# Kernel optimization log

Hardware: AMD Instinct MI355X
Metric: run time of the kernel (lower is better)

## Reference

```python
import jax, jax.numpy as jnp
import numpy as np

D_IN, H, NH = 256, 512, 8
B, T = 8, 1024


def sinusoidal_pe(seq_len, d_model):
    pos = jnp.arange(seq_len, dtype=jnp.float32)[:, None]
    div = jnp.exp(jnp.arange(0, d_model, 2, dtype=jnp.float32) * (-jnp.log(10000.0) / d_model))
    pe = jnp.zeros((seq_len, d_model), jnp.float32)
    pe = pe.at[:, 0::2].set(jnp.sin(pos * div)).at[:, 1::2].set(jnp.cos(pos * div))
    return pe


def layer_norm(x, g, b, eps=1e-5):
    mu = jnp.mean(x, -1, keepdims=True)
    var = jnp.mean((x - mu) ** 2, -1, keepdims=True)
    return (x - mu) * jax.lax.rsqrt(var + eps) * g + b


def lstm_dir(x, wih, whh, bih, bhh):
    # x: [B,T,H]; wih/whh: [4H,H]; gate order i,f,g,o (PyTorch convention)
    Bx = x.shape[0]
    Hh = whh.shape[1]
    xg = jnp.einsum('bth,gh->btg', x, wih) + bih  # precompute input gates [B,T,4H]

    def step(carry, xg_t):
        h, c = carry
        gates = xg_t + h @ whh.T + bhh
        i, f, g, o = jnp.split(gates, 4, axis=-1)
        c = jax.nn.sigmoid(f) * c + jax.nn.sigmoid(i) * jnp.tanh(g)
        h = jax.nn.sigmoid(o) * jnp.tanh(c)
        return (h, c), h

    h0 = jnp.zeros((Bx, Hh), x.dtype)
    _, hs = jax.lax.scan(step, (h0, h0), xg.transpose(1, 0, 2))
    return hs.transpose(1, 0, 2)  # [B,T,H]


def setup_inputs():
    key = jax.random.key(0)
    ks = jax.random.split(key, 30)
    s = 0.02

    def g(k, shape):
        return jax.random.normal(k, shape, jnp.float32) * s

    return {
        'temporal_data': jax.random.normal(ks[0], (B, T, D_IN), jnp.float32),
        'w_in': g(ks[1], (H, D_IN)), 'b_in': jnp.zeros((H,), jnp.float32),
        'wq': g(ks[2], (H, H)), 'bq': jnp.zeros((H,), jnp.float32),
        'wk': g(ks[3], (H, H)), 'bk': jnp.zeros((H,), jnp.float32),
        'wv': g(ks[4], (H, H)), 'bv': jnp.zeros((H,), jnp.float32),
        'wo': g(ks[5], (H, H)), 'bo': jnp.zeros((H,), jnp.float32),
        'g1': jnp.ones((H,), jnp.float32), 'b1': jnp.zeros((H,), jnp.float32),
        'wih_f': g(ks[6], (4 * H, H)), 'whh_f': g(ks[7], (4 * H, H)),
        'bih_f': jnp.zeros((4 * H,), jnp.float32), 'bhh_f': jnp.zeros((4 * H,), jnp.float32),
        'wih_b': g(ks[8], (4 * H, H)), 'whh_b': g(ks[9], (4 * H, H)),
        'bih_b': jnp.zeros((4 * H,), jnp.float32), 'bhh_b': jnp.zeros((4 * H,), jnp.float32),
        'g2': jnp.ones((2 * H,), jnp.float32), 'b2': jnp.zeros((2 * H,), jnp.float32),
        'w_out': g(ks[10], (H, 2 * H)), 'b_out': jnp.zeros((H,), jnp.float32),
    }


def reference(temporal_data, w_in, b_in, wq, bq, wk, bk, wv, bv, wo, bo, g1, b1,
              wih_f, whh_f, bih_f, bhh_f, wih_b, whh_b, bih_b, bhh_b, g2, b2, w_out, b_out):
    x = temporal_data @ w_in.T + b_in                      # [B,T,H]
    Bx, Tx, _ = x.shape
    x = x + sinusoidal_pe(Tx, H)
    residual = x

    hd = H // NH
    q = (x @ wq.T + bq).reshape(Bx, Tx, NH, hd).transpose(0, 2, 1, 3)
    k = (x @ wk.T + bk).reshape(Bx, Tx, NH, hd).transpose(0, 2, 1, 3)
    v = (x @ wv.T + bv).reshape(Bx, Tx, NH, hd).transpose(0, 2, 1, 3)
    scores = jnp.einsum('bhqd,bhkd->bhqk', q, k) * (hd ** -0.5)
    causal = jnp.triu(jnp.ones((Tx, Tx), bool), 1)
    scores = jnp.where(causal, jnp.float32(-1e9), scores)
    attn = jax.nn.softmax(scores, axis=-1)
    o = jnp.einsum('bhqk,bhkd->bhqd', attn, v).transpose(0, 2, 1, 3).reshape(Bx, Tx, H)
    o = o @ wo.T + bo

    x = layer_norm(o + residual, g1, b1)                   # dropout in eval = identity

    h_fwd = lstm_dir(x, wih_f, whh_f, bih_f, bhh_f)
    h_bwd = jnp.flip(lstm_dir(jnp.flip(x, 1), wih_b, whh_b, bih_b, bhh_b), 1)
    lstm_out = jnp.concatenate([h_fwd, h_bwd], axis=-1)    # [B,T,2H]
    lstm_out = layer_norm(lstm_out, g2, b2)

    emb = jnp.mean(lstm_out, axis=1)                       # [B,2H]
    return emb @ w_out.T + b_out                           # [B,H]
```

## Files before the change

### kernel.cpp

```cpp
#include <hip/hip_runtime.h>

typedef unsigned short u16;
typedef unsigned int   u32;
typedef unsigned long long u64;
typedef __attribute__((ext_vector_type(8))) short short8v;
typedef __attribute__((ext_vector_type(4))) float f32x4;
typedef __attribute__((ext_vector_type(4))) unsigned int u32x4;

#define DINL __device__ __forceinline__

DINL u16 f2bf(float f){ union{float f;u32 u;} v{f}; return (u16)((v.u + 0x7fffu + ((v.u>>16)&1u))>>16); }
DINL float bf2f(u16 b){ union{u32 u;float f;} v{(u32)b<<16}; return v.f; }
DINL f32x4 MFMA16(short8v a, short8v b, f32x4 c){ return __builtin_amdgcn_mfma_f32_16x16x32_bf16(a,b,c,0,0,0); }
DINL void gl16(const void* g, void* l){
  __builtin_amdgcn_global_load_lds((const __attribute__((address_space(1))) void*)g,
                                   (__attribute__((address_space(3))) void*)l, 16, 0, 0);
}
DINL float wredd(float v){
#pragma unroll
  for (int m=1;m<64;m<<=1) v += __shfl_xor(v, m);
  return v;
}
DINL float sigm(float x){ return 1.f/(1.f+__expf(-x)); }
DINL float tanh_(float x){ return 2.f/(1.f+__expf(-2.f*x)) - 1.f; }

__global__ __launch_bounds__(256) void zerok(u32* __restrict__ dst){
  size_t i = ((size_t)blockIdx.x*256 + threadIdx.x)*4;
  u32x4 z = {0,0,0,0};
  *(u32x4*)(dst + i) = z;
}

__global__ __launch_bounds__(256) void cvtk(const float* __restrict__ src, u16* __restrict__ dst, int n){
  int i = (blockIdx.x*256 + threadIdx.x)*4;
  float4 v = *(const float4*)(src + i);
  dst[i+0]=f2bf(v.x); dst[i+1]=f2bf(v.y); dst[i+2]=f2bf(v.z); dst[i+3]=f2bf(v.w);
}

template<int EPI>
__global__ __launch_bounds__(256) void gemm128(
    const u16* __restrict__ A, const u16* __restrict__ W,
    const float* __restrict__ bias0, const float* __restrict__ bias1, const float* __restrict__ bias2,
    const u16* __restrict__ resid, u16* __restrict__ out, int M, int N, int K)
{
  __shared__ __align__(16) u16 Al[128*64];
  __shared__ __align__(16) u16 Bl[128*64];
  const int tid = threadIdx.x, lane = tid & 63, w = tid >> 6;
  const int wr = w >> 1, wc = w & 1;
  const int m0 = blockIdx.y * 128, n0 = blockIdx.x * 128;
  f32x4 acc[4][4] = {};
  for (int k0 = 0; k0 < K; k0 += 64) {
#pragma unroll
    for (int j = 0; j < 4; ++j) {
      int idx = (j*4 + w)*64 + lane;
      int r = idx >> 3, c8 = idx & 7;
      gl16(A + (size_t)(m0 + r)*K + k0 + c8*8, (void*)(Al + (size_t)(j*4+w)*512));
      gl16(W + (size_t)(n0 + r)*K + k0 + c8*8, (void*)(Bl + (size_t)(j*4+w)*512));
    }
    __syncthreads();
#pragma unroll
    for (int kk = 0; kk < 2; ++kk) {
      short8v af[4], bf[4];
#pragma unroll
      for (int i = 0; i < 4; ++i)
        af[i] = *(const short8v*)(Al + ((wr*64 + i*16 + (lane&15))*64 + kk*32 + (lane>>4)*8));
#pragma unroll
      for (int i = 0; i < 4; ++i)
        bf[i] = *(const short8v*)(Bl + ((wc*64 + i*16 + (lane&15))*64 + kk*32 + (lane>>4)*8));
#pragma unroll
      for (int mi=0;mi<4;++mi)
#pragma unroll
        for (int ni=0;ni<4;++ni)
          acc[mi][ni] = MFMA16(af[mi], bf[ni], acc[mi][ni]);
    }
    __syncthreads();
  }
#pragma unroll
  for (int mi=0;mi<4;++mi)
#pragma unroll
    for (int ni=0;ni<4;++ni)
#pragma unroll
      for (int r=0;r<4;++r) {
        int m = m0 + wr*64 + mi*16 + (lane>>4)*4 + r;
        int n = n0 + wc*64 + ni*16 + (lane&15);
        float v = acc[mi][ni][r];
        if constexpr (EPI == 0) {
          int t = m & 1023;
          float ang = (float)t * expf((float)(n & ~1) * (-9.210340371976184f/512.f));
          v += bias0[n] + ((n & 1) ? cosf(ang) : sinf(ang));
          out[(size_t)m*512 + n] = f2bf(v);
        } else if constexpr (EPI == 1) {
          int g = n >> 9, n5 = n & 511, hh = n5 >> 6, dh = n5 & 63;
          v += (g==0 ? bias0 : g==1 ? bias1 : bias2)[n5];
          size_t bh = (size_t)((m>>10)*8 + hh);
          u16 val = f2bf(v);
          if (g == 0)      out[(bh*1024 + (m&1023))*64 + dh] = val;
          else if (g == 1) out[4194304 + (bh*1024 + (m&1023))*64 + dh] = val;
          else             out[8388608 + (bh*64 + dh)*1024 + (m&1023)] = val;
        } else {
          v += bias0[n] + bf2f(resid[(size_t)m*512 + n]);
          out[(size_t)m*512 + n] = f2bf(v);
        }
      }
}

__global__ __launch_bounds__(256) void attnk(const u16* __restrict__ qb, const u16* __restrict__ kb,
                                             const u16* __restrict__ vt, u16* __restrict__ attno)
{
  __shared__ __align__(16) u16 P[4][16][72];
  const int tid = threadIdx.x, lane = tid & 63, w = tid >> 6;
  const int bh = blockIdx.x >> 4, qblk = blockIdx.x & 15;
  const int b = bh >> 3, h = bh & 7;
  const float scale = 0.125f;
  short8v qf[2];
  {
    const u16* qbase = qb + ((size_t)bh*1024 + qblk*64 + w*16)*64;
#pragma unroll
    for (int kk=0;kk<2;++kk)
      qf[kk] = *(const short8v*)(qbase + (size_t)(lane&15)*64 + kk*32 + (lane>>4)*8);
  }
  f32x4 o[4] = {};
  float mrun[4], lrun[4];
#pragma unroll
  for (int r=0;r<4;++r){ mrun[r] = -1e30f; lrun[r] = 0.f; }
  for (int kblk = 0; kblk <= qblk; ++kblk) {
    f32x4 s[4] = {};
#pragma unroll
    for (int kk=0;kk<2;++kk)
#pragma unroll
      for (int nt=0;nt<4;++nt) {
        short8v kf = *(const short8v*)(kb + ((size_t)bh*1024 + kblk*64 + nt*16 + (lane&15))*64 + kk*32 + (lane>>4)*8);
        s[nt] = MFMA16(qf[kk], kf, s[nt]);
      }
    float pnew[4][4];
#pragma unroll
    for (int r=0;r<4;++r) {
      int q = qblk*64 + w*16 + (lane>>4)*4 + r;
      float sv[4]; float rowmax = -1e30f;
#pragma unroll
      for (int nt=0;nt<4;++nt) {
        int key = kblk*64 + nt*16 + (lane&15);
        float x = s[nt][r]*scale;
        if (key > q) x = -1e30f;
        sv[nt] = x; rowmax = fmaxf(rowmax, x);
      }
#pragma unroll
      for (int msk=1; msk<16; msk<<=1) rowmax = fmaxf(rowmax, __shfl_xor(rowmax, msk));
      float mnew = fmaxf(mrun[r], rowmax);
      float sf = __expf(mrun[r]-mnew);
      float psum = 0.f;
#pragma unroll
      for (int nt=0;nt<4;++nt){ float p = __expf(sv[nt]-mnew); pnew[nt][r]=p; psum += p; }
#pragma unroll
      for (int msk=1; msk<16; msk<<=1) psum += __shfl_xor(psum, msk);
      lrun[r] = lrun[r]*sf + psum;
      mrun[r] = mnew;
#pragma unroll
      for (int nt=0;nt<4;++nt) o[nt][r] *= sf;
    }
#pragma unroll
    for (int nt=0;nt<4;++nt)
#pragma unroll
      for (int r=0;r<4;++r)
        P[w][(lane>>4)*4+r][nt*16+(lane&15)] = f2bf(pnew[nt][r]);
#pragma unroll
    for (int kk=0;kk<2;++kk) {
      short8v pf = *(const short8v*)&P[w][lane&15][kk*32 + (lane>>4)*8];
#pragma unroll
      for (int nt=0;nt<4;++nt) {
        short8v vf = *(const short8v*)(vt + ((size_t)bh*64 + nt*16 + (lane&15))*1024 + kblk*64 + kk*32 + (lane>>4)*8);
        o[nt] = MFMA16(pf, vf, o[nt]);
      }
    }
  }
#pragma unroll
  for (int nt=0;nt<4;++nt)
#pragma unroll
    for (int r=0;r<4;++r) {
      int q = qblk*64 + w*16 + (lane>>4)*4 + r;
      int dh = nt*16 + (lane&15);
      attno[((size_t)b*1024 + q)*512 + h*64 + dh] = f2bf(o[nt][r] / lrun[r]);
    }
}

__global__ __launch_bounds__(256) void ln1k(const u16* __restrict__ pre, const float* __restrict__ g1,
                                            const float* __restrict__ b1, u16* __restrict__ xl){
  int row = blockIdx.x*4 + (threadIdx.x>>6), lane = threadIdx.x&63;
  short8v xv = *(const short8v*)(pre + (size_t)row*512 + lane*8);
  float v[8], s=0.f, s2=0.f;
#pragma unroll
  for (int e=0;e<8;++e){ v[e]=bf2f((u16)xv[e]); s+=v[e]; s2+=v[e]*v[e]; }
  s = wredd(s); s2 = wredd(s2);
  float mu = s*(1.f/512.f);
  float rs = rsqrtf(s2*(1.f/512.f) - mu*mu + 1e-5f);
  int b = row>>10, t = row&1023;
  short8v ov;
#pragma unroll
  for (int e=0;e<8;++e){ int c=lane*8+e; ov[e]=(short)f2bf((v[e]-mu)*rs*g1[c]+b1[c]); }
  *(short8v*)(xl + ((size_t)t*8 + b)*512 + lane*8) = ov;
}

__global__ __launch_bounds__(512, 2) void lstmk(
    const u16* __restrict__ xl,
    const float* __restrict__ wih_f, const float* __restrict__ whh_f,
    const float* __restrict__ bih_f, const float* __restrict__ bhh_f,
    const float* __restrict__ wih_b, const float* __restrict__ whh_b,
    const float* __restrict__ bih_b, const float* __restrict__ bhh_b,
    u32* __restrict__ hx, u16* __restrict__ hs)
{
  extern __shared__ float RED[];

  const int tid = threadIdx.x, lane = tid&63, w = tid>>6;
  const int d = blockIdx.x >> 4, slice = blockIdx.x & 15, u0 = slice*32;
  const float* WIHg = d ? wih_b : wih_f;
  const float* WHHg = d ? whh_b : whh_f;
  const float* BIH  = d ? bih_b : bih_f;
  const float* BHH  = d ? bhh_b : bhh_f;

  const int l15 = lane&15, l16 = lane>>4;

  short8v wi[8][2], wh[8][2];
#pragma unroll
  for (int nt=0; nt<8; ++nt) {
    const int g = nt>>1, uh = nt&1;
    const size_t row = (size_t)(g*512 + u0 + uh*16 + l15);
#pragma unroll
    for (int kk=0; kk<2; ++kk) {
      const int k = w*64 + kk*32 + l16*8;
      const float* pi = WIHg + row*512 + k;
      const float* ph = WHHg + row*512 + k;
      float4 a0 = *(const float4*)pi, a1 = *(const float4*)(pi+4);
      float4 b0 = *(const float4*)ph, b1 = *(const float4*)(ph+4);
      short8v si, sh;
      si[0]=(short)f2bf(a0.x); si[1]=(short)f2bf(a0.y); si[2]=(short)f2bf(a0.z); si[3]=(short)f2bf(a0.w);
      si[4]=(short)f2bf(a1.x); si[5]=(short)f2bf(a1.y); si[6]=(short)f2bf(a1.z); si[7]=(short)f2bf(a1.w);
      sh[0]=(short)f2bf(b0.x); sh[1]=(short)f2bf(b0.y); sh[2]=(short)f2bf(b0.z); sh[3]=(short)f2bf(b0.w);
      sh[4]=(short)f2bf(b1.x); sh[5]=(short)f2bf(b1.y); sh[6]=(short)f2bf(b1.z); sh[7]=(short)f2bf(b1.w);
      wi[nt][kk] = si; wh[nt][kk] = sh;
    }
  }

  const bool act = tid < 256;
  const int b_ = tid>>5, u_ = tid&31;
  float c_state = 0.f, bias_c[4];
  if (act)
#pragma unroll
    for (int g=0;g<4;++g) bias_c[g] = BIH[g*512+u0+u_] + BHH[g*512+u0+u_];

  __syncthreads();

  for (int t = 0; t < 1024; ++t) {
    const int te = d ? 1023 - t : t;
    f32x4 acc[8] = {};
    {
      const u16* xb = xl + ((size_t)te*8 + (lane&7))*512 + w*64 + l16*8;
      short8v xf0 = *(const short8v*)(xb);
      short8v xf1 = *(const short8v*)(xb + 32);
#pragma unroll
      for (int nt=0; nt<8; ++nt) acc[nt] = MFMA16(xf0, wi[nt][0], acc[nt]);
#pragma unroll
      for (int nt=0; nt<8; ++nt) acc[nt] = MFMA16(xf1, wi[nt][1], acc[nt]);
    }
    if (t > 0) {
      const u32 tg = (u32)t;
      const u32* pb = hx + ((size_t)d*2 + ((t-1)&1))*4096 + (size_t)(lane&7)*512 + w*64 + l16*8;
      u32x4 q0,q1,q2,q3;
      for (;;) {
        asm volatile(
          "global_load_dwordx4 %0, %4, off sc0 sc1\n\t"
          "global_load_dwordx4 %1, %4, off offset:16 sc0 sc1\n\t"
          "global_load_dwordx4 %2, %4, off offset:128 sc0 sc1\n\t"
          "global_load_dwordx4 %3, %4, off offset:144 sc0 sc1\n\t"
          "s_waitcnt vmcnt(0)"
          : "=&v"(q0),"=&v"(q1),"=&v"(q2),"=&v"(q3)
          : "v"(pb));
        bool ok = true;
#pragma unroll
        for (int e=0;e<4;++e) {
          ok = ok && ((q0[e]&0xffffu)==tg) && ((q1[e]&0xffffu)==tg)
                  && ((q2[e]&0xffffu)==tg) && ((q3[e]&0xffffu)==tg);
        }
        if (__all(ok)) break;
        __builtin_amdgcn_s_sleep(1);
      }
      short8v hf0, hf1;
#pragma unroll
      for (int e=0;e<4;++e) {
        hf0[e]   = (short)(q0[e] >> 16);
        hf0[4+e] = (short)(q1[e] >> 16);
        hf1[e]   = (short)(q2[e] >> 16);
        hf1[4+e] = (short)(q3[e] >> 16);
      }
#pragma unroll
      for (int nt=0; nt<8; ++nt) acc[nt] = MFMA16(hf0, wh[nt][0], acc[nt]);
#pragma unroll
      for (int nt=0; nt<8; ++nt) acc[nt] = MFMA16(hf1, wh[nt][1], acc[nt]);
    }
    float* R = RED + (size_t)(t & 1)*8192;
    if (lane < 32)
#pragma unroll
      for (int nt=0; nt<8; ++nt)
        *(f32x4*)(R + ((size_t)(w*8+nt)*32 + lane)*4) = acc[nt];
    __syncthreads();
    if (act) {
      const int lc = (u_&15) + 16*(b_>>2), rg = b_&3, uh = u_>>4;
      float gates[4];
#pragma unroll
      for (int g=0;g<4;++g) {
        float s = 0.f;
#pragma unroll
        for (int wv=0; wv<8; ++wv) s += R[((size_t)(wv*8 + g*2 + uh)*32 + lc)*4 + rg];
        gates[g] = s + bias_c[g];
      }
      float ig = sigm(gates[0]), fg = sigm(gates[1]), gg = tanh_(gates[2]), og = sigm(gates[3]);
      c_state = fg*c_state + ig*gg;
      u16 hv = f2bf(og * tanh_(c_state));
      hs[((size_t)(d*1024 + te)*8 + b_)*512 + u0 + u_] = hv;
      u32 word = ((u32)hv << 16) | (u32)(t + 1);
      u32* dst = hx + ((size_t)d*2 + (t&1))*4096 + (size_t)b_*512 + u0 + u_;
      asm volatile("global_store_dword %0, %1, off sc0 sc1" :: "v"(dst), "v"(word) : "memory");
    }
  }
}

__global__ __launch_bounds__(256) void ln2k(const u16* __restrict__ hs, const float* __restrict__ g2,
                                            const float* __restrict__ b2, float* __restrict__ emb){
  __shared__ float accl[4][1024];
  int b = blockIdx.x>>4, chunk = blockIdx.x&15;
  int lane = threadIdx.x&63, w = threadIdx.x>>6;
  for (int i=lane;i<1024;i+=64) accl[w][i]=0.f;
#pragma unroll 1
  for (int i=0;i<16;++i) {
    int t = chunk*64 + w*16 + i;
    short8v xf = *(const short8v*)(hs + ((size_t)t*8 + b)*512 + lane*8);
    short8v xb = *(const short8v*)(hs + ((size_t)(1024+t)*8 + b)*512 + lane*8);
    float vf[8], vb[8], s=0.f, s2=0.f;
#pragma unroll
    for (int e=0;e<8;++e){ vf[e]=bf2f((u16)xf[e]); vb[e]=bf2f((u16)xb[e]);
                           s += vf[e]+vb[e]; s2 += vf[e]*vf[e]+vb[e]*vb[e]; }
    s = wredd(s); s2 = wredd(s2);
    float mu = s*(1.f/1024.f);
    float rs = rsqrtf(s2*(1.f/1024.f) - mu*mu + 1e-5f);
#pragma unroll
    for (int e=0;e<8;++e){
      int c = lane*8+e;
      accl[w][c]     += (vf[e]-mu)*rs*g2[c]     + b2[c];
      accl[w][512+c] += (vb[e]-mu)*rs*g2[512+c] + b2[512+c];
    }
  }
  __syncthreads();
  for (int c = threadIdx.x; c < 1024; c += 256)
    atomicAdd(emb + (size_t)b*1024 + c, accl[0][c]+accl[1][c]+accl[2][c]+accl[3][c]);
}

__global__ __launch_bounds__(256) void fink(const float* __restrict__ emb, const float* __restrict__ w_out,
                                            const float* __restrict__ b_out, float* __restrict__ out){
  int gid = blockIdx.x*256 + threadIdx.x;
  int n = gid>>3, b = gid&7;
  const float* e = emb + (size_t)b*1024;
  const float* wr = w_out + (size_t)n*1024;
  float s = 0.f;
  for (int k=0;k<1024;k+=4) {
    float4 ev = *(const float4*)(e+k);
    float4 wv = *(const float4*)(wr+k);
    s += ev.x*wv.x + ev.y*wv.y + ev.z*wv.z + ev.w*wv.w;
  }
  out[(size_t)b*512 + n] = b_out[n] + s*(1.f/1024.f);
}

#define OFF_EMB   0u
#define OFF_HX    32768u
#define OFF_A0    98304u
#define OFF_WIN   4292608u
#define OFF_WQKV  4554752u
#define OFF_WO    6127616u
#define OFF_X0B   6651904u
#define OFF_QB    15040512u
#define OFF_PRE   15040512u
#define OFF_XL    23429120u
#define OFF_ATT   40206336u
#define OFF_HS    48594944u

extern "C" void kernel_launch(void* const* d_in, const int* in_sizes, int n_in,
                              void* d_out, int out_size, void* d_ws, size_t ws_size,
                              hipStream_t stream) {
  const float* temporal = (const float*)d_in[0];
  const float* w_in = (const float*)d_in[1];  const float* b_in = (const float*)d_in[2];
  const float* wq = (const float*)d_in[3];    const float* bq = (const float*)d_in[4];
  const float* wk = (const float*)d_in[5];    const float* bk = (const float*)d_in[6];
  const float* wv = (const float*)d_in[7];    const float* bv = (const float*)d_in[8];
  const float* wo = (const float*)d_in[9];    const float* bo = (const float*)d_in[10];
  const float* g1 = (const float*)d_in[11];   const float* b1 = (const float*)d_in[12];
  const float* wih_f = (const float*)d_in[13]; const float* whh_f = (const float*)d_in[14];
  const float* bih_f = (const float*)d_in[15]; const float* bhh_f = (const float*)d_in[16];
  const float* wih_b = (const float*)d_in[17]; const float* whh_b = (const float*)d_in[18];
  const float* bih_b = (const float*)d_in[19]; const float* bhh_b = (const float*)d_in[20];
  const float* g2 = (const float*)d_in[21];   const float* b2 = (const float*)d_in[22];
  const float* w_out = (const float*)d_in[23]; const float* b_out = (const float*)d_in[24];

  char* ws = (char*)d_ws;
  float* EMB = (float*)(ws + OFF_EMB);
  u32* HX   = (u32*)(ws + OFF_HX);
  u16* A0   = (u16*)(ws + OFF_A0);
  u16* WIN  = (u16*)(ws + OFF_WIN);
  u16* WQKV = (u16*)(ws + OFF_WQKV);
  u16* WOb  = (u16*)(ws + OFF_WO);
  u16* X0B  = (u16*)(ws + OFF_X0B);
  u16* QB   = (u16*)(ws + OFF_QB);
  u16* PRE  = (u16*)(ws + OFF_PRE);
  u16* XL   = (u16*)(ws + OFF_XL);
  u16* ATT  = (u16*)(ws + OFF_ATT);
  u16* HS   = (u16*)(ws + OFF_HS);

  (void)hipFuncSetAttribute((const void*)lstmk, hipFuncAttributeMaxDynamicSharedMemorySize, 65536);

  zerok<<<24,256,0,stream>>>((u32*)(ws + OFF_EMB));

  cvtk<<<2048,256,0,stream>>>(temporal, A0, 2097152);
  cvtk<<<128, 256,0,stream>>>(w_in, WIN, 131072);
  cvtk<<<256, 256,0,stream>>>(wq, WQKV,           262144);
  cvtk<<<256, 256,0,stream>>>(wk, WQKV + 262144,  262144);
  cvtk<<<256, 256,0,stream>>>(wv, WQKV + 524288,  262144);
  cvtk<<<256, 256,0,stream>>>(wo, WOb, 262144);

  gemm128<0><<<dim3(4,64), 256, 0, stream>>>(A0, WIN, b_in, nullptr, nullptr, nullptr, X0B, 8192, 512, 256);
  gemm128<1><<<dim3(12,64),256, 0, stream>>>(X0B, WQKV, bq, bk, bv, nullptr, QB, 8192, 1536, 512);
  attnk<<<1024,256,0,stream>>>(QB, QB + 4194304, QB + 8388608, ATT);
  gemm128<3><<<dim3(4,64), 256, 0, stream>>>(ATT, WOb, bo, nullptr, nullptr, X0B, PRE, 8192, 512, 512);
  ln1k<<<2048,256,0,stream>>>(PRE, g1, b1, XL);
  lstmk<<<32,512,65536,stream>>>(XL, wih_f, whh_f, bih_f, bhh_f, wih_b, whh_b, bih_b, bhh_b, HX, HS);
  ln2k<<<128,256,0,stream>>>(HS, g2, b2, EMB);
  fink<<<16,256,0,stream>>>(EMB, w_out, b_out, (float*)d_out);
}
```

Baseline: 3.399 ms.

## Prefetch LSTM hidden-state poll before input MFMAs and pad reduction LDS layout

The first poll of the previous step's hidden-state words is issued as relaxed agent-scope atomic loads before the input-gate MFMAs, so the cross-block exchange latency overlaps compute instead of being serialized after it. The LDS partial-sum layout is changed to a padded stride-9 layout that puts the eight warp partials next to each other, which is meant to cut bank conflicts in the gate reduction, with a tree-shaped sum. The launch bound drops the 2-blocks hint and shared memory grows to fit the padding. Relaxed atomics replace the explicit sc0 sc1 cache-bypass loads, which may change visibility behaviour in the spin loop.

```diff
diff --git a/kernel.cpp b/kernel.cpp
--- a/kernel.cpp
+++ b/kernel.cpp
@@ -199,7 +199,7 @@
   *(short8v*)(xl + ((size_t)t*8 + b)*512 + lane*8) = ov;
 }
 
-__global__ __launch_bounds__(512, 2) void lstmk(
+__global__ __launch_bounds__(512) void lstmk(
     const u16* __restrict__ xl,
     const float* __restrict__ wih_f, const float* __restrict__ whh_f,
     const float* __restrict__ bih_f, const float* __restrict__ bhh_f,
@@ -250,6 +250,15 @@
 
   for (int t = 0; t < 1024; ++t) {
     const int te = d ? 1023 - t : t;
+    u64 pv[8];
+    const u64* pb = (const u64*)(hx + ((size_t)d*2 + ((t-1)&1))*4096
+                                    + (size_t)(lane&7)*512 + w*64 + l16*8);
+    if (t > 0) {
+#pragma unroll
+      for (int j=0;j<4;++j) pv[j]   = __hip_atomic_load(pb+j,    __ATOMIC_RELAXED, __HIP_MEMORY_SCOPE_AGENT);
+#pragma unroll
+      for (int j=0;j<4;++j) pv[4+j] = __hip_atomic_load(pb+16+j, __ATOMIC_RELAXED, __HIP_MEMORY_SCOPE_AGENT);
+    }
     f32x4 acc[8] = {};
     {
       const u16* xb = xl + ((size_t)te*8 + (lane&7))*512 + w*64 + l16*8;
@@ -262,54 +271,46 @@
     }
     if (t > 0) {
       const u32 tg = (u32)t;
-      const u32* pb = hx + ((size_t)d*2 + ((t-1)&1))*4096 + (size_t)(lane&7)*512 + w*64 + l16*8;
-      u32x4 q0,q1,q2,q3;
       for (;;) {
-        asm volatile(
-          "global_load_dwordx4 %0, %4, off sc0 sc1\n\t"
-          "global_load_dwordx4 %1, %4, off offset:16 sc0 sc1\n\t"
-          "global_load_dwordx4 %2, %4, off offset:128 sc0 sc1\n\t"
-          "global_load_dwordx4 %3, %4, off offset:144 sc0 sc1\n\t"
-          "s_waitcnt vmcnt(0)"
-          : "=&v"(q0),"=&v"(q1),"=&v"(q2),"=&v"(q3)
-          : "v"(pb));
         bool ok = true;
 #pragma unroll
-        for (int e=0;e<4;++e) {
-          ok = ok && ((q0[e]&0xffffu)==tg) && ((q1[e]&0xffffu)==tg)
-                  && ((q2[e]&0xffffu)==tg) && ((q3[e]&0xffffu)==tg);
-        }
+        for (int j=0;j<8;++j)
+          ok = ok && ((u32)(pv[j] & 0xffffu) == tg) && ((u32)((pv[j]>>32) & 0xffffu) == tg);
         if (__all(ok)) break;
         __builtin_amdgcn_s_sleep(1);
+#pragma unroll
+        for (int j=0;j<4;++j) pv[j]   = __hip_atomic_load(pb+j,    __ATOMIC_RELAXED, __HIP_MEMORY_SCOPE_AGENT);
+#pragma unroll
+        for (int j=0;j<4;++j) pv[4+j] = __hip_atomic_load(pb+16+j, __ATOMIC_RELAXED, __HIP_MEMORY_SCOPE_AGENT);
       }
       short8v hf0, hf1;
 #pragma unroll
-      for (int e=0;e<4;++e) {
-        hf0[e]   = (short)(q0[e] >> 16);
-        hf0[4+e] = (short)(q1[e] >> 16);
-        hf1[e]   = (short)(q2[e] >> 16);
-        hf1[4+e] = (short)(q3[e] >> 16);
+      for (int j=0;j<4;++j) {
+        hf0[2*j]   = (short)(u32)(pv[j]   >> 16);
+        hf0[2*j+1] = (short)(pv[j]   >> 48);
+        hf1[2*j]   = (short)(u32)(pv[4+j] >> 16);
+        hf1[2*j+1] = (short)(pv[4+j] >> 48);
       }
 #pragma unroll
       for (int nt=0; nt<8; ++nt) acc[nt] = MFMA16(hf0, wh[nt][0], acc[nt]);
 #pragma unroll
       for (int nt=0; nt<8; ++nt) acc[nt] = MFMA16(hf1, wh[nt][1], acc[nt]);
     }
-    float* R = RED + (size_t)(t & 1)*8192;
+    float* R = RED + (size_t)(t & 1)*9216;
     if (lane < 32)
 #pragma unroll
       for (int nt=0; nt<8; ++nt)
-        *(f32x4*)(R + ((size_t)(w*8+nt)*32 + lane)*4) = acc[nt];
+#pragma unroll
+        for (int rg=0; rg<4; ++rg)
+          R[(((size_t)nt*4 + rg)*32 + lane)*9 + w] = acc[nt][rg];
     __syncthreads();
     if (act) {
-      const int lc = (u_&15) + 16*(b_>>2), rg = b_&3, uh = u_>>4;
+      const int uh = u_>>4, lc = (u_&15) + 16*(b_>>2), rg = b_&3;
       float gates[4];
 #pragma unroll
       for (int g=0;g<4;++g) {
-        float s = 0.f;
-#pragma unroll
-        for (int wv=0; wv<8; ++wv) s += R[((size_t)(wv*8 + g*2 + uh)*32 + lc)*4 + rg];
-        gates[g] = s + bias_c[g];
+        const float* q = R + (((size_t)(g*2+uh)*4 + rg)*32 + lc)*9;
+        gates[g] = ((q[0]+q[1])+(q[2]+q[3])) + ((q[4]+q[5])+(q[6]+q[7])) + bias_c[g];
       }
       float ig = sigm(gates[0]), fg = sigm(gates[1]), gg = tanh_(gates[2]), og = sigm(gates[3]);
       c_state = fg*c_state + ig*gg;
@@ -411,7 +412,7 @@
   u16* ATT  = (u16*)(ws + OFF_ATT);
   u16* HS   = (u16*)(ws + OFF_HS);
 
-  (void)hipFuncSetAttribute((const void*)lstmk, hipFuncAttributeMaxDynamicSharedMemorySize, 65536);
+  (void)hipFuncSetAttribute((const void*)lstmk, hipFuncAttributeMaxDynamicSharedMemorySize, 73728);
 
   zerok<<<24,256,0,stream>>>((u32*)(ws + OFF_EMB));
 
@@ -427,7 +428,7 @@
   attnk<<<1024,256,0,stream>>>(QB, QB + 4194304, QB + 8388608, ATT);
   gemm128<3><<<dim3(4,64), 256, 0, stream>>>(ATT, WOb, bo, nullptr, nullptr, X0B, PRE, 8192, 512, 512);
   ln1k<<<2048,256,0,stream>>>(PRE, g1, b1, XL);
-  lstmk<<<32,512,65536,stream>>>(XL, wih_f, whh_f, bih_f, bhh_f, wih_b, whh_b, bih_b, bhh_b, HX, HS);
+  lstmk<<<32,512,73728,stream>>>(XL, wih_f, whh_f, bih_f, bhh_f, wih_b, whh_b, bih_b, bhh_b, HX, HS);
   ln2k<<<128,256,0,stream>>>(HS, g2, b2, EMB);
   fink<<<16,256,0,stream>>>(EMB, w_out, b_out, (float*)d_out);
 }
```

After: 7.568 ms. 123% more time.
